# Performance work log

Measured on AMD Instinct MI355X. Metric: run time of the kernel, lower is better.

The kernel has to match this reference:

```python
import jax, jax.numpy as jnp
import numpy as np

IH, IW = 32, 32
HEADS = 8
DIM_HEAD = 64
SCALE = DIM_HEAD ** -0.5


def _make_relative_index():
    # Matches torch buffer: ceil Euclidean distance between all pairs of 2D coords.
    ii, jj = np.meshgrid(np.arange(IH), np.arange(IW), indexing='ij')
    coords = np.stack([ii.ravel(), jj.ravel()])  # [2, n]
    rel = coords[:, :, None] - coords[:, None, :]  # [2, n, n]
    dist = np.ceil(np.sqrt(rel[0] ** 2 + rel[1] ** 2))
    return jnp.asarray(dist.astype(np.int32).ravel())  # [n*n]


def setup_inputs() -> dict:
    key = jax.random.key(0)
    k1, k2, k3, k4 = jax.random.split(key, 4)
    b, n, inp = 32, IH * IW, 512
    inner = HEADS * DIM_HEAD
    diag = int(np.ceil(np.sqrt((IH - 1) ** 2 + (IW - 1) ** 2)))
    return {
        'x': jax.random.normal(k1, (b, n, inp), jnp.float32),
        'w_qkv': jax.random.normal(k2, (inp, inner * 3), jnp.float32) * (inp ** -0.5),
        'bias_table': jax.random.normal(k3, (diag + 1, HEADS), jnp.float32) * 0.02,
        'w_out': jax.random.normal(k4, (inner, 512), jnp.float32) * (inner ** -0.5),
        'b_out': jnp.zeros((512,), jnp.float32),
        'relative_index': _make_relative_index(),
    }


def reference(x, w_qkv, bias_table, w_out, b_out, relative_index):
    b, n, _ = x.shape
    qkv = x @ w_qkv  # [b, n, 3*inner]
    q, k, v = jnp.split(qkv, 3, axis=-1)
    def to_heads(t):
        return t.reshape(b, n, HEADS, DIM_HEAD).transpose(0, 2, 1, 3)  # b h n d
    q, k, v = to_heads(q), to_heads(k), to_heads(v)
    dots = jnp.einsum('bhid,bhjd->bhij', q, k) * SCALE  # [b, h, n, n]
    # gather relative bias: [n*n, h] -> [1, h, n, n]
    rel_bias = bias_table[relative_index].reshape(n, n, HEADS).transpose(2, 0, 1)
    attn = jax.nn.softmax(dots + rel_bias[None], axis=-1)
    out = jnp.einsum('bhij,bhjd->bhid', attn, v)  # b h n d
    out = out.transpose(0, 2, 1, 3).reshape(b, n, HEADS * DIM_HEAD)
    return out @ w_out + b_out
```

## Files before the change

### kernel.cpp

```cpp
#include <hip/hip_runtime.h>
#include <hip/hip_bf16.h>
#include <cstdint>

typedef __bf16 bf16_t;
typedef bf16_t bf16x8 __attribute__((ext_vector_type(8)));
typedef float f32x4 __attribute__((ext_vector_type(4)));
typedef float f32x16 __attribute__((ext_vector_type(16)));
typedef unsigned u32x4 __attribute__((ext_vector_type(4)));

#define MFMA16(a, b, c) __builtin_amdgcn_mfma_f32_16x16x32_bf16(a, b, c, 0, 0, 0)
#define MFMA32(a, b, c) __builtin_amdgcn_mfma_f32_32x32x16_bf16(a, b, c, 0, 0, 0)

#define GLOAD_LDS16(g, l)                                                  \
    __builtin_amdgcn_global_load_lds(                                      \
        (const __attribute__((address_space(1))) unsigned*)(g),            \
        (__attribute__((address_space(3))) unsigned*)(l), 16, 0, 0)

constexpr int LDK = 72;

#define QSCALE 0.1803368801f
#define LOG2E 1.44269504f

__global__ void zero_out(unsigned short* __restrict__ out, long n) {
    long i = (long)blockIdx.x * 256 + threadIdx.x;
    if (i < n) out[i] = 0;
}

__global__ void detect_dtype(const unsigned* __restrict__ x,
                             int* __restrict__ flag) {
    if (threadIdx.x == 0 && blockIdx.x == 0) {
        int cnt = 0;
        for (int i = 0; i < 1024; ++i) {
            unsigned e = (x[i] >> 7) & 0xFF;
            cnt += (e > 100 && e < 150) ? 1 : 0;
        }
        *flag = (cnt > 512) ? 1 : 0;
    }
}

__global__ __launch_bounds__(256) void convert_x(const void* __restrict__ in,
                                                 bf16_t* __restrict__ out,
                                                 const int* __restrict__ flagp) {
    const int fl = *flagp;
    long i = ((long)blockIdx.x * 256 + threadIdx.x) * 8;
    if (fl) {
        *(bf16x8*)&out[i] = *(const bf16x8*)&((const bf16_t*)in)[i];
    } else {
        f32x4 lo = *(const f32x4*)&((const float*)in)[i];
        f32x4 hi = *(const f32x4*)&((const float*)in)[i + 4];
        bf16x8 v;
#pragma unroll
        for (int e = 0; e < 4; ++e) {
            v[e] = (bf16_t)lo[e];
            v[e + 4] = (bf16_t)hi[e];
        }
        *(bf16x8*)&out[i] = v;
    }
}

__global__ void transpose_flex(const void* __restrict__ in,
                               bf16_t* __restrict__ out, int R, int C,
                               const int* __restrict__ flagp, int scale_rows) {
    const int fl = *flagp;
    __shared__ bf16_t tile[32][33];
    int c0 = blockIdx.x * 32, r0 = blockIdx.y * 32;
    int x = threadIdx.x, y = threadIdx.y;
#pragma unroll
    for (int i = 0; i < 4; ++i) {
        long idx = (long)(r0 + y + 8 * i) * C + c0 + x;
        float fv = fl ? (float)((const bf16_t*)in)[idx]
                      : ((const float*)in)[idx];
        if (c0 + x < scale_rows) fv *= QSCALE;
        tile[y + 8 * i][x] = (bf16_t)fv;
    }
    __syncthreads();
#pragma unroll
    for (int i = 0; i < 4; ++i)
        out[(long)(c0 + y + 8 * i) * R + r0 + x] = tile[x][y + 8 * i];
}

__global__ __launch_bounds__(256) void build_bias_perm(
    const int* __restrict__ rel_index, const void* __restrict__ bias_table,
    float* __restrict__ perm, const int* __restrict__ flagp) {
    const int fl = *flagp;
    const int jt = blockIdx.x;
    const int qb = blockIdx.y;
    const int t = threadIdx.x;
    const int lane = t & 63;
    const int h = (t >> 6) + 4 * blockIdx.z;
    const int i = qb * 32 + (lane & 31);
    const int hi = lane >> 5;
    float out[16];
#pragma unroll
    for (int r = 0; r < 16; ++r) {
        int j = jt * 32 + (r & 3) + 8 * (r >> 2) + 4 * hi;
        int ridx = rel_index[i * 1024 + j];
        ridx = ridx < 0 ? 0 : (ridx > 44 ? 44 : ridx);
        float bv = fl ? (float)((const bf16_t*)bias_table)[ridx * 8 + h]
                      : ((const float*)bias_table)[ridx * 8 + h];
        out[r] = bv * LOG2E;
    }
    long off = (((long)(h * 32 + qb) * 32 + jt) << 10) + lane * 16;
#pragma unroll
    for (int g = 0; g < 4; ++g)
        *(f32x4*)&perm[off + 4 * g] = *(f32x4*)&out[4 * g];
}

__global__ __launch_bounds__(256) void transpose_v(
    const bf16_t* __restrict__ qkv, bf16_t* __restrict__ vt) {
    __shared__ bf16_t tile[64 * 64];
    const int jt = blockIdx.x;
    const int bh = blockIdx.y;
    const int b = bh >> 3, h = bh & 7;
    const bf16_t* src = qkv + (long)b * 1024 * 1536 + 1024 + h * 64;
    const int t = threadIdx.x;
    const int r = t >> 3, c8 = t & 7;
    const int j0 = jt * 64;
#pragma unroll
    for (int rep = 0; rep < 2; ++rep) {
        int jj = r + 32 * rep;
        *(bf16x8*)&tile[jj * 64 + ((c8 ^ (jj >> 3)) << 3)] =
            *(const bf16x8*)&src[(long)(j0 + jj) * 1536 + c8 * 8];
    }
    __syncthreads();
#pragma unroll
    for (int rep = 0; rep < 2; ++rep) {
        int dd = r + 32 * rep;
        int jc = c8 * 8;
        bf16_t o[8];
#pragma unroll
        for (int e = 0; e < 8; ++e) {
            int row = jc + e;
            o[e] = tile[row * 64 + (((dd >> 3) ^ (row >> 3)) << 3) + (dd & 7)];
        }
        *(bf16x8*)&vt[((long)bh << 16) + (long)dd * 1024 + j0 + jc] =
            *(bf16x8*)&o[0];
    }
}

template <bool BIAS, bool OUTFLEX>
__global__ __launch_bounds__(256) void gemm_lds(
    const bf16_t* __restrict__ A, const bf16_t* __restrict__ Bt, int K,
    int lda, long a_row0, void* __restrict__ C, int ldc, long c_row0,
    const void* __restrict__ bias, const int* __restrict__ flagp) {
    const int fl = *flagp;
    __shared__ bf16_t a_lds[128 * 64];
    __shared__ bf16_t b_lds[128 * 64];
    int t = threadIdx.x;
    int wave = t >> 6, lane = t & 63;
    int m16 = lane & 15, quad = lane >> 4;
    int wr = wave >> 1, wc = wave & 1;
    long m0 = (long)blockIdx.y * 128;
    int n0 = blockIdx.x * 128;

    f32x4 acc[4][4] = {};

    for (int ks = 0; ks < K; ks += 64) {
#pragma unroll
        for (int i = 0; i < 4; ++i) {
            int c = wave * 256 + i * 64 + lane;
            int row = c >> 3, kc = (c & 7) << 3;
            GLOAD_LDS16(&A[(a_row0 + m0 + row) * (long)lda + ks + kc],
                        &a_lds[row * 64 + kc]);
            GLOAD_LDS16(&Bt[(long)(n0 + row) * K + ks + kc],
                        &b_lds[row * 64 + kc]);
        }
        __syncthreads();
#pragma unroll
        for (int kf = 0; kf < 2; ++kf) {
            bf16x8 af[4], bfr[4];
#pragma unroll
            for (int mb = 0; mb < 4; ++mb)
                af[mb] = *(const bf16x8*)&a_lds[(wr * 64 + mb * 16 + m16) * 64 +
                                                kf * 32 + quad * 8];
#pragma unroll
            for (int nb = 0; nb < 4; ++nb)
                bfr[nb] = *(const bf16x8*)&b_lds[(wc * 64 + nb * 16 + m16) * 64 +
                                                 kf * 32 + quad * 8];
#pragma unroll
            for (int mb = 0; mb < 4; ++mb)
#pragma unroll
                for (int nb = 0; nb < 4; ++nb)
                    acc[mb][nb] = MFMA16(af[mb], bfr[nb], acc[mb][nb]);
        }
        __syncthreads();
    }

#pragma unroll
    for (int mb = 0; mb < 4; ++mb) {
#pragma unroll
        for (int nb = 0; nb < 4; ++nb) {
            int col = n0 + wc * 64 + nb * 16 + m16;
#pragma unroll
            for (int r = 0; r < 4; ++r) {
                long row = m0 + wr * 64 + mb * 16 + quad * 4 + r;
                float v = acc[mb][nb][r];
                if (BIAS) {
                    float bb = fl ? (float)((const bf16_t*)bias)[col]
                                  : ((const float*)bias)[col];
                    v += bb;
                }
                long off = (c_row0 + row) * (long)ldc + col;
                if (OUTFLEX && !fl)
                    ((float*)C)[off] = v;
                else
                    ((bf16_t*)C)[off] = (bf16_t)v;
            }
        }
    }
}

template <bool AFLEX, bool BIAS, bool OUTFLEX>
__global__ __launch_bounds__(256) void gemm128(
    const void* __restrict__ A, const bf16_t* __restrict__ Bt, int K, int lda,
    long a_row0, void* __restrict__ C, int ldc, long c_row0,
    const void* __restrict__ bias, const int* __restrict__ flagp) {
    const int fl = *flagp;
    __shared__ bf16_t a_lds[128 * LDK];
    __shared__ bf16_t b_lds[128 * LDK];
    int t = threadIdx.x;
    int wave = t >> 6, lane = t & 63;
    int m16 = lane & 15, quad = lane >> 4;
    int wr = wave >> 1, wc = wave & 1;
    long m0 = (long)blockIdx.y * 128;
    int n0 = blockIdx.x * 128;

    f32x4 acc[4][4] = {};

    for (int ks = 0; ks < K; ks += 64) {
#pragma unroll
        for (int i = 0; i < 4; ++i) {
            int c = t + 256 * i;
            int row = c >> 3;
            int kc = (c & 7) << 3;
            bf16x8 av;
            if (AFLEX && !fl) {
                const float* Af = (const float*)A;
                long base = (a_row0 + m0 + row) * (long)lda + ks + kc;
                f32x4 lo = *(const f32x4*)&Af[base];
                f32x4 hi = *(const f32x4*)&Af[base + 4];
#pragma unroll
                for (int e = 0; e < 4; ++e) {
                    av[e] = (bf16_t)lo[e];
                    av[e + 4] = (bf16_t)hi[e];
                }
            } else {
                av = *(const bf16x8*)&(
                    (const bf16_t*)A)[(a_row0 + m0 + row) * (long)lda + ks + kc];
            }
            *(bf16x8*)&a_lds[row * LDK + kc] = av;
            *(bf16x8*)&b_lds[row * LDK + kc] =
                *(const bf16x8*)&Bt[(long)(n0 + row) * K + ks + kc];
        }
        __syncthreads();
#pragma unroll
        for (int kf = 0; kf < 2; ++kf) {
            bf16x8 af[4], bfr[4];
#pragma unroll
            for (int mb = 0; mb < 4; ++mb)
                af[mb] = *(const bf16x8*)&a_lds[(wr * 64 + mb * 16 + m16) * LDK +
                                                kf * 32 + quad * 8];
#pragma unroll
            for (int nb = 0; nb < 4; ++nb)
                bfr[nb] = *(const bf16x8*)&b_lds[(wc * 64 + nb * 16 + m16) * LDK +
                                                 kf * 32 + quad * 8];
#pragma unroll
            for (int mb = 0; mb < 4; ++mb)
#pragma unroll
                for (int nb = 0; nb < 4; ++nb)
                    acc[mb][nb] = MFMA16(af[mb], bfr[nb], acc[mb][nb]);
        }
        __syncthreads();
    }

#pragma unroll
    for (int mb = 0; mb < 4; ++mb) {
#pragma unroll
        for (int nb = 0; nb < 4; ++nb) {
            int col = n0 + wc * 64 + nb * 16 + m16;
#pragma unroll
            for (int r = 0; r < 4; ++r) {
                long row = m0 + wr * 64 + mb * 16 + quad * 4 + r;
                float v = acc[mb][nb][r];
                if (BIAS) {
                    float bb = fl ? (float)((const bf16_t*)bias)[col]
                                  : ((const float*)bias)[col];
                    v += bb;
                }
                long off = (c_row0 + row) * (long)ldc + col;
                if (OUTFLEX && !fl)
                    ((float*)C)[off] = v;
                else
                    ((bf16_t*)C)[off] = (bf16_t)v;
            }
        }
    }
}

__global__ __launch_bounds__(256, 2) void flash_attn3(
    bf16_t* __restrict__ qkv, const bf16_t* __restrict__ vt,
    const float* __restrict__ bias_perm) {
    __shared__ bf16_t k_lds[2][64 * 64];
    __shared__ bf16_t v_lds[2][64 * 64];

    const int t = threadIdx.x;
    const int lane = t & 63, wave = t >> 6;
    const int l31 = lane & 31, hi = lane >> 5;
    const int h = blockIdx.x;
    const int b = blockIdx.z;
    bf16_t* base = qkv + (long)b * 1024 * 1536;
    bf16_t* qb = base + h * 64;
    const bf16_t* kb = base + 512 + h * 64;
    const bf16_t* vtb = vt + ((long)(b * 8 + h) << 16);
    const int qblkA = blockIdx.y * 4 + wave;
    const int qblkB = qblkA + 16;
    const int q0A = qblkA * 32, q0B = qblkB * 32;
    const float* bpA = bias_perm + (((long)(h * 32 + qblkA)) << 15) + lane * 16;
    const float* bpB = bias_perm + (((long)(h * 32 + qblkB)) << 15) + lane * 16;

    bf16x8 qfA[4], qfB[4];
#pragma unroll
    for (int s = 0; s < 4; ++s) {
        qfA[s] = *(const bf16x8*)&qb[(long)(q0A + l31) * 1536 + s * 16 + hi * 8];
        qfB[s] = *(const bf16x8*)&qb[(long)(q0B + l31) * 1536 + s * 16 + hi * 8];
    }

    f32x16 oacc0A = {}, oacc1A = {}, laccA = {};
    f32x16 oacc0B = {}, oacc1B = {}, laccB = {};
    bf16x8 ones;
#pragma unroll
    for (int e = 0; e < 8; ++e) ones[e] = (bf16_t)1.0f;

    const int srow = t >> 3, pc = t & 7;
    const int kc0 = (pc ^ (srow & 7)) << 3;

    {
        GLOAD_LDS16(&kb[(long)srow * 1536 + kc0],
                    &k_lds[0][srow * 64 + pc * 8]);
        GLOAD_LDS16(&kb[(long)(srow + 32) * 1536 + kc0],
                    &k_lds[0][(srow + 32) * 64 + pc * 8]);
        GLOAD_LDS16(&vtb[(long)srow * 1024 + kc0],
                    &v_lds[0][srow * 64 + pc * 8]);
        GLOAD_LDS16(&vtb[(long)(srow + 32) * 1024 + kc0],
                    &v_lds[0][(srow + 32) * 64 + pc * 8]);
    }
    __syncthreads();

#define SOFTMAX_REPACK(S, DW)                                              \
    {                                                                      \
        float sv_[16];                                                     \
        _Pragma("unroll") for (int r = 0; r < 16; ++r)                     \
            sv_[r] = __builtin_amdgcn_exp2f((S)[r]);                       \
        _Pragma("unroll") for (int g = 0; g < 4; ++g) {                    \
            unsigned da_, db_;                                             \
            asm("v_cvt_pk_bf16_f32 %0, %1, %2"                             \
                : "=v"(da_) : "v"(sv_[4 * g]), "v"(sv_[4 * g + 1]));       \
            asm("v_cvt_pk_bf16_f32 %0, %1, %2"                             \
                : "=v"(db_) : "v"(sv_[4 * g + 2]), "v"(sv_[4 * g + 3]));   \
            (DW)[2 * g] = da_;                                             \
            (DW)[2 * g + 1] = db_;                                         \
        }                                                                  \
        _Pragma("unroll") for (int kk = 0; kk < 2; ++kk) {                 \
            asm("v_permlane32_swap_b32 %0, %1"                             \
                : "+v"((DW)[4 * kk + 0]), "+v"((DW)[4 * kk + 2]));         \
            asm("v_permlane32_swap_b32 %0, %1"                             \
                : "+v"((DW)[4 * kk + 1]), "+v"((DW)[4 * kk + 3]));         \
        }                                                                  \
    }

#define PACK_PA(DW, KK)                                                    \
    __builtin_bit_cast(bf16x8, (u32x4){(DW)[4 * (KK) + 0],                 \
                                       (DW)[4 * (KK) + 1],                 \
                                       (DW)[4 * (KK) + 2],                 \
                                       (DW)[4 * (KK) + 3]})

    for (int tt = 0; tt < 16; ++tt) {
        const int cur = tt & 1;
        const float* btA = bpA + ((long)tt << 11);
        const float* btB = bpB + ((long)tt << 11);
        f32x4 bA0[4], bB0[4];
#pragma unroll
        for (int g = 0; g < 4; ++g) {
            bA0[g] = *(const f32x4*)(btA + 4 * g);
            bB0[g] = *(const f32x4*)(btB + 4 * g);
        }
        if (tt < 15) {
            const int nb = cur ^ 1;
            long j0n = (long)(tt + 1) * 64;
            GLOAD_LDS16(&kb[(j0n + srow) * 1536 + kc0],
                        &k_lds[nb][srow * 64 + pc * 8]);
            GLOAD_LDS16(&kb[(j0n + srow + 32) * 1536 + kc0],
                        &k_lds[nb][(srow + 32) * 64 + pc * 8]);
            GLOAD_LDS16(&vtb[(long)srow * 1024 + j0n + kc0],
                        &v_lds[nb][srow * 64 + pc * 8]);
            GLOAD_LDS16(&vtb[(long)(srow + 32) * 1024 + j0n + kc0],
                        &v_lds[nb][(srow + 32) * 64 + pc * 8]);
        }

        f32x4 bA1[4], bB1[4];
#pragma unroll
        for (int js = 0; js < 2; ++js) {
            const int krow = js * 32 + l31;
            bf16x8 kf[4];
#pragma unroll
            for (int st = 0; st < 4; ++st)
                kf[st] = *(const bf16x8*)&k_lds[cur][krow * 64 +
                          (((st * 2 + hi) ^ (krow & 7)) << 3)];
            f32x16 sA, sB;
#pragma unroll
            for (int g = 0; g < 4; ++g) {
                const f32x4 ba = js ? bA1[g] : bA0[g];
                const f32x4 bb = js ? bB1[g] : bB0[g];
#pragma unroll
                for (int e = 0; e < 4; ++e) {
                    sA[4 * g + e] = ba[e];
                    sB[4 * g + e] = bb[e];
                }
            }
            __builtin_amdgcn_s_setprio(1);
#pragma unroll
            for (int st = 0; st < 4; ++st) sA = MFMA32(kf[st], qfA[st], sA);
#pragma unroll
            for (int st = 0; st < 4; ++st) sB = MFMA32(kf[st], qfB[st], sB);
            __builtin_amdgcn_s_setprio(0);
            if (js == 0) {
#pragma unroll
                for (int g = 0; g < 4; ++g) {
                    bA1[g] = *(const f32x4*)(btA + 1024 + 4 * g);
                    bB1[g] = *(const f32x4*)(btB + 1024 + 4 * g);
                }
            }
            unsigned dwA[8], dwB[8];
            SOFTMAX_REPACK(sA, dwA);
            SOFTMAX_REPACK(sB, dwB);
            __builtin_amdgcn_s_setprio(1);
#pragma unroll
            for (int kk = 0; kk < 2; ++kk) {
                bf16x8 paA = PACK_PA(dwA, kk);
                bf16x8 paB = PACK_PA(dwB, kk);
                const int vr0 = l31, vr1 = 32 + l31;
                bf16x8 vf0 = *(const bf16x8*)&v_lds[cur][vr0 * 64 +
                              (((js * 4 + kk * 2 + hi) ^ (vr0 & 7)) << 3)];
                bf16x8 vf1 = *(const bf16x8*)&v_lds[cur][vr1 * 64 +
                              (((js * 4 + kk * 2 + hi) ^ (vr1 & 7)) << 3)];
                laccA = MFMA32(paA, ones, laccA);
                oacc0A = MFMA32(paA, vf0, oacc0A);
                oacc1A = MFMA32(paA, vf1, oacc1A);
                laccB = MFMA32(paB, ones, laccB);
                oacc0B = MFMA32(paB, vf0, oacc0B);
                oacc1B = MFMA32(paB, vf1, oacc1B);
            }
            __builtin_amdgcn_s_setprio(0);
        }
        __syncthreads();
    }

#pragma unroll
    for (int r = 0; r < 16; ++r) {
        int row = (r & 3) + 8 * (r >> 2) + 4 * hi;
        float invA = 1.0f / laccA[r];
        float invB = 1.0f / laccB[r];
        qb[(long)(q0A + row) * 1536 + l31] = (bf16_t)(oacc0A[r] * invA);
        qb[(long)(q0A + row) * 1536 + 32 + l31] = (bf16_t)(oacc1A[r] * invA);
        qb[(long)(q0B + row) * 1536 + l31] = (bf16_t)(oacc0B[r] * invB);
        qb[(long)(q0B + row) * 1536 + 32 + l31] = (bf16_t)(oacc1B[r] * invB);
    }
}

__global__ __launch_bounds__(256) void flash_attn2(
    bf16_t* __restrict__ qkv, const float* __restrict__ bias_perm) {
    __shared__ bf16_t k_lds[2][64 * 64];
    __shared__ bf16_t v_lds[2][64 * 64];

    const int t = threadIdx.x;
    const int lane = t & 63, wave = t >> 6;
    const int l31 = lane & 31, hi = lane >> 5;
    const int h = blockIdx.x;
    const int b = blockIdx.z;
    bf16_t* base = qkv + (long)b * 1024 * 1536;
    bf16_t* qb = base + h * 64;
    const bf16_t* kb = base + 512 + h * 64;
    const bf16_t* vb = base + 1024 + h * 64;
    const int qblk = blockIdx.y * 4 + wave;
    const int q0w = qblk * 32;
    const float* bp = bias_perm + (((long)(h * 32 + qblk)) << 15) + lane * 16;

    bf16x8 qf[4];
#pragma unroll
    for (int s = 0; s < 4; ++s)
        qf[s] = *(const bf16x8*)&qb[(long)(q0w + l31) * 1536 + s * 16 + hi * 8];

    f32x16 oacc0 = {}, oacc1 = {}, lacc = {};
    bf16x8 ones;
#pragma unroll
    for (int e = 0; e < 8; ++e) ones[e] = (bf16_t)1.0f;

    const int sr0 = t >> 3, sg0 = t & 7;
    const int sr1 = sr0 + 32;

    {
        bf16x8 k0 = *(const bf16x8*)&kb[(long)sr0 * 1536 + sg0 * 8];
        bf16x8 k1 = *(const bf16x8*)&kb[(long)sr1 * 1536 + sg0 * 8];
        bf16x8 v0 = *(const bf16x8*)&vb[(long)sr0 * 1536 + sg0 * 8];
        bf16x8 v1 = *(const bf16x8*)&vb[(long)sr1 * 1536 + sg0 * 8];
        *(bf16x8*)&k_lds[0][sr0 * 64 + ((sg0 ^ (sr0 & 7)) << 3)] = k0;
        *(bf16x8*)&k_lds[0][sr1 * 64 + ((sg0 ^ (sr1 & 7)) << 3)] = k1;
#pragma unroll
        for (int e = 0; e < 8; ++e) {
            int d0 = sg0 * 8 + e;
            v_lds[0][d0 * 64 + (((sr0 >> 3) ^ (d0 & 7)) << 3) + (sr0 & 7)] = v0[e];
            v_lds[0][d0 * 64 + (((sr1 >> 3) ^ (d0 & 7)) << 3) + (sr1 & 7)] = v1[e];
        }
    }
    __syncthreads();

    for (int tt = 0; tt < 16; ++tt) {
        const int cur = tt & 1;
        bf16x8 kn0 = {}, kn1 = {}, vn0 = {}, vn1 = {};
        if (tt < 15) {
            long j0n = (long)(tt + 1) * 64;
            kn0 = *(const bf16x8*)&kb[(j0n + sr0) * 1536 + sg0 * 8];
            kn1 = *(const bf16x8*)&kb[(j0n + sr1) * 1536 + sg0 * 8];
            vn0 = *(const bf16x8*)&vb[(j0n + sr0) * 1536 + sg0 * 8];
            vn1 = *(const bf16x8*)&vb[(j0n + sr1) * 1536 + sg0 * 8];
        }
        const float* bt = bp + ((long)tt << 11);
        f32x4 bv[8];
        bv[0] = *(const f32x4*)(bt);
        bv[1] = *(const f32x4*)(bt + 4);
        bv[2] = *(const f32x4*)(bt + 8);
        bv[3] = *(const f32x4*)(bt + 12);
        bv[4] = *(const f32x4*)(bt + 1024);
        bv[5] = *(const f32x4*)(bt + 1028);
        bv[6] = *(const f32x4*)(bt + 1032);
        bv[7] = *(const f32x4*)(bt + 1036);

#pragma unroll
        for (int js = 0; js < 2; ++js) {
            f32x16 s;
#pragma unroll
            for (int g = 0; g < 4; ++g) {
#pragma unroll
                for (int e = 0; e < 4; ++e) s[4 * g + e] = bv[4 * js + g][e];
            }
            const int krow = js * 32 + l31;
#pragma unroll
            for (int st = 0; st < 4; ++st) {
                bf16x8 kf = *(const bf16x8*)&k_lds[cur][krow * 64 +
                             (((st * 2 + hi) ^ (krow & 7)) << 3)];
                s = MFMA32(kf, qf[st], s);
            }
            float sv[16];
#pragma unroll
            for (int r = 0; r < 16; ++r)
                sv[r] = __builtin_amdgcn_exp2f(s[r]);
            unsigned dw[8];
#pragma unroll
            for (int g = 0; g < 4; ++g) {
                unsigned da, db;
                asm("v_cvt_pk_bf16_f32 %0, %1, %2"
                    : "=v"(da) : "v"(sv[4 * g]), "v"(sv[4 * g + 1]));
                asm("v_cvt_pk_bf16_f32 %0, %1, %2"
                    : "=v"(db) : "v"(sv[4 * g + 2]), "v"(sv[4 * g + 3]));
                dw[2 * g] = da;
                dw[2 * g + 1] = db;
            }
#pragma unroll
            for (int kk = 0; kk < 2; ++kk) {
                asm("v_permlane32_swap_b32 %0, %1"
                    : "+v"(dw[4 * kk + 0]), "+v"(dw[4 * kk + 2]));
                asm("v_permlane32_swap_b32 %0, %1"
                    : "+v"(dw[4 * kk + 1]), "+v"(dw[4 * kk + 3]));
            }
#pragma unroll
            for (int kk = 0; kk < 2; ++kk) {
                u32x4 uv;
                uv[0] = dw[4 * kk + 0];
                uv[1] = dw[4 * kk + 1];
                uv[2] = dw[4 * kk + 2];
                uv[3] = dw[4 * kk + 3];
                bf16x8 pa = __builtin_bit_cast(bf16x8, uv);
                lacc = MFMA32(pa, ones, lacc);
#pragma unroll
                for (int db2 = 0; db2 < 2; ++db2) {
                    const int vrow = db2 * 32 + l31;
                    bf16x8 vf = *(const bf16x8*)&v_lds[cur][vrow * 64 +
                                 (((js * 4 + kk * 2 + hi) ^ (vrow & 7)) << 3)];
                    if (db2 == 0)
                        oacc0 = MFMA32(pa, vf, oacc0);
                    else
                        oacc1 = MFMA32(pa, vf, oacc1);
                }
            }
        }
        if (tt < 15) {
            const int nb = cur ^ 1;
            *(bf16x8*)&k_lds[nb][sr0 * 64 + ((sg0 ^ (sr0 & 7)) << 3)] = kn0;
            *(bf16x8*)&k_lds[nb][sr1 * 64 + ((sg0 ^ (sr1 & 7)) << 3)] = kn1;
#pragma unroll
            for (int e = 0; e < 8; ++e) {
                int d0 = sg0 * 8 + e;
                v_lds[nb][d0 * 64 + (((sr0 >> 3) ^ (d0 & 7)) << 3) + (sr0 & 7)] =
                    vn0[e];
                v_lds[nb][d0 * 64 + (((sr1 >> 3) ^ (d0 & 7)) << 3) + (sr1 & 7)] =
                    vn1[e];
            }
        }
        __syncthreads();
    }

#pragma unroll
    for (int r = 0; r < 16; ++r) {
        float inv = 1.0f / lacc[r];
        int row = (r & 3) + 8 * (r >> 2) + 4 * hi;
        qb[(long)(q0w + row) * 1536 + l31] = (bf16_t)(oacc0[r] * inv);
        qb[(long)(q0w + row) * 1536 + 32 + l31] = (bf16_t)(oacc1[r] * inv);
    }
}

extern "C" void kernel_launch(void* const* d_in, const int* in_sizes, int n_in,
                              void* d_out, int out_size, void* d_ws,
                              size_t ws_size, hipStream_t stream) {
    const void* x = nullptr;
    const void* w_qkv = nullptr;
    const void* bias_table = nullptr;
    const void* w_out = nullptr;
    const void* b_out = nullptr;
    const void* rel_raw = nullptr;
    for (int i = 0; i < n_in; ++i) {
        switch (in_sizes[i]) {
            case 16777216: x = d_in[i]; break;
            case 786432:  w_qkv = d_in[i]; break;
            case 360:     bias_table = d_in[i]; break;
            case 262144:  w_out = d_in[i]; break;
            case 512:     b_out = d_in[i]; break;
            case 1048576: rel_raw = d_in[i]; break;
            default: break;
        }
    }
    if (!x || !w_qkv || !bias_table || !w_out || !b_out || !rel_raw) {
        x = d_in[0]; w_qkv = d_in[1]; bias_table = d_in[2];
        w_out = d_in[3]; b_out = d_in[4]; rel_raw = d_in[5];
    }
    const int* rel_index = (const int*)rel_raw;

    char* ws = (char*)d_ws;
    bf16_t* wqkvT = (bf16_t*)ws;
    bf16_t* woutT = (bf16_t*)(ws + 1572864);
    int* flag = (int*)(ws + 1572864 + 524288);
    float* rel_bias = (float*)(ws + 1572864 + 524288 + 256);
    const size_t fixed = 1572864 + 524288 + 256 + 33554432;
    const size_t xbf_bytes = (size_t)32 * 1024 * 512 * sizeof(bf16_t);
    const size_t qkv_pb = (size_t)1024 * 1536 * sizeof(bf16_t);
    const size_t vt_pb = (size_t)8 * 64 * 1024 * sizeof(bf16_t);

    if (ws_size < fixed + qkv_pb) {
        long n = (long)out_size;
        long nblk = (n + 255) / 256;
        if (nblk > 0)
            zero_out<<<(unsigned)nblk, 256, 0, stream>>>(
                (unsigned short*)d_out, n);
        return;
    }

    bool have_xbf = ws_size >= fixed + xbf_bytes + qkv_pb;
    bool have_vt = ws_size >= fixed + xbf_bytes + qkv_pb + vt_pb;
    bf16_t* x_bf = (bf16_t*)(ws + fixed);
    bf16_t* qkv = have_xbf ? (bf16_t*)(ws + fixed + xbf_bytes)
                           : (bf16_t*)(ws + fixed);

    size_t avail = ws_size - fixed - (have_xbf ? xbf_bytes : 0);
    size_t pb = have_vt ? (qkv_pb + vt_pb) : qkv_pb;
    int chunk = (int)(avail / pb);
    if (chunk > 32) chunk = 32;
    if (chunk < 1) chunk = 1;
    while (32 % chunk) --chunk;
    bf16_t* vt = (bf16_t*)((char*)qkv + (size_t)chunk * qkv_pb);

    detect_dtype<<<1, 64, 0, stream>>>((const unsigned*)x, flag);
    transpose_flex<<<dim3(1536 / 32, 512 / 32), dim3(32, 8), 0, stream>>>(
        w_qkv, wqkvT, 512, 1536, flag, 512);
    transpose_flex<<<dim3(512 / 32, 512 / 32), dim3(32, 8), 0, stream>>>(
        w_out, woutT, 512, 512, flag, 0);
    build_bias_perm<<<dim3(32, 32, 2), 256, 0, stream>>>(
        rel_index, bias_table, rel_bias, flag);
    if (have_xbf)
        convert_x<<<8192, 256, 0, stream>>>(x, x_bf, flag);

    for (int b0 = 0; b0 < 32; b0 += chunk) {
        long row0 = (long)b0 * 1024;
        int mrows = chunk * 1024;
        if (have_xbf) {
            gemm_lds<false, false>
                <<<dim3(1536 / 128, mrows / 128), 256, 0, stream>>>(
                    x_bf, wqkvT, 512, 512, row0, qkv, 1536, 0, nullptr, flag);
        } else {
            gemm128<true, false, false>
                <<<dim3(1536 / 128, mrows / 128), 256, 0, stream>>>(
                    x, wqkvT, 512, 512, row0, qkv, 1536, 0, nullptr, flag);
        }
        if (have_vt) {
            transpose_v<<<dim3(16, chunk * 8), 256, 0, stream>>>(qkv, vt);
            flash_attn3<<<dim3(8, 4, chunk), 256, 0, stream>>>(qkv, vt,
                                                               rel_bias);
        } else {
            flash_attn2<<<dim3(8, 8, chunk), 256, 0, stream>>>(qkv, rel_bias);
        }
        gemm_lds<true, true>
            <<<dim3(512 / 128, mrows / 128), 256, 0, stream>>>(
                qkv, woutT, 512, 1536, 0, d_out, 512, row0, b_out, flag);
    }
}
```

Baseline: 461.9 us.

## Fuse V transpose into QKV GEMM epilogue and triple-buffer attention K/V loads

The QKV projection GEMM now writes the V columns directly in transposed layout into the vt buffer, which removes the separate transpose_v kernel and its extra read/write pass over V. The flash attention kernel moves from a double-buffered to a triple-buffered K/V LDS pipeline: it prefetches two tiles ahead, uses raw s_waitcnt/s_barrier instead of __syncthreads, and hoists the second-half bias loads. It also drops the occupancy hint of 2 blocks per CU. The larger LDS footprint and the missing occupancy hint may cut blocks per CU, and the uint2 transposed stores from the GEMM epilogue are narrow and strided.

```diff
diff --git a/kernel.cpp b/kernel.cpp
--- a/kernel.cpp
+++ b/kernel.cpp
@@ -106,43 +106,12 @@
         *(f32x4*)&perm[off + 4 * g] = *(f32x4*)&out[4 * g];
 }
 
-__global__ __launch_bounds__(256) void transpose_v(
-    const bf16_t* __restrict__ qkv, bf16_t* __restrict__ vt) {
-    __shared__ bf16_t tile[64 * 64];
-    const int jt = blockIdx.x;
-    const int bh = blockIdx.y;
-    const int b = bh >> 3, h = bh & 7;
-    const bf16_t* src = qkv + (long)b * 1024 * 1536 + 1024 + h * 64;
-    const int t = threadIdx.x;
-    const int r = t >> 3, c8 = t & 7;
-    const int j0 = jt * 64;
-#pragma unroll
-    for (int rep = 0; rep < 2; ++rep) {
-        int jj = r + 32 * rep;
-        *(bf16x8*)&tile[jj * 64 + ((c8 ^ (jj >> 3)) << 3)] =
-            *(const bf16x8*)&src[(long)(j0 + jj) * 1536 + c8 * 8];
-    }
-    __syncthreads();
-#pragma unroll
-    for (int rep = 0; rep < 2; ++rep) {
-        int dd = r + 32 * rep;
-        int jc = c8 * 8;
-        bf16_t o[8];
-#pragma unroll
-        for (int e = 0; e < 8; ++e) {
-            int row = jc + e;
-            o[e] = tile[row * 64 + (((dd >> 3) ^ (row >> 3)) << 3) + (dd & 7)];
-        }
-        *(bf16x8*)&vt[((long)bh << 16) + (long)dd * 1024 + j0 + jc] =
-            *(bf16x8*)&o[0];
-    }
-}
-
-template <bool BIAS, bool OUTFLEX>
+template <bool BIAS, bool OUTFLEX, bool VSPLIT>
 __global__ __launch_bounds__(256) void gemm_lds(
     const bf16_t* __restrict__ A, const bf16_t* __restrict__ Bt, int K,
     int lda, long a_row0, void* __restrict__ C, int ldc, long c_row0,
-    const void* __restrict__ bias, const int* __restrict__ flagp) {
+    const void* __restrict__ bias, bf16_t* __restrict__ vtout,
+    const int* __restrict__ flagp) {
     const int fl = *flagp;
     __shared__ bf16_t a_lds[128 * 64];
     __shared__ bf16_t b_lds[128 * 64];
@@ -191,20 +160,33 @@
 #pragma unroll
         for (int nb = 0; nb < 4; ++nb) {
             int col = n0 + wc * 64 + nb * 16 + m16;
-#pragma unroll
-            for (int r = 0; r < 4; ++r) {
-                long row = m0 + wr * 64 + mb * 16 + quad * 4 + r;
-                float v = acc[mb][nb][r];
-                if (BIAS) {
-                    float bb = fl ? (float)((const bf16_t*)bias)[col]
-                                  : ((const float*)bias)[col];
-                    v += bb;
+            long rowb = m0 + wr * 64 + mb * 16 + quad * 4;
+            if (VSPLIT && col >= 1024) {
+                int dd = col - 1024;
+                bf16_t ov[4];
+#pragma unroll
+                for (int r = 0; r < 4; ++r) ov[r] = (bf16_t)acc[mb][nb][r];
+                long bb_ = rowb >> 10;
+                long jj = rowb & 1023;
+                *(uint2*)&vtout[((bb_ * 8 + (dd >> 6)) << 16) +
+                                (long)(dd & 63) * 1024 + jj] =
+                    *(const uint2*)&ov[0];
+            } else {
+#pragma unroll
+                for (int r = 0; r < 4; ++r) {
+                    long row = rowb + r;
+                    float v = acc[mb][nb][r];
+                    if (BIAS) {
+                        float bb = fl ? (float)((const bf16_t*)bias)[col]
+                                      : ((const float*)bias)[col];
+                        v += bb;
+                    }
+                    long off = (c_row0 + row) * (long)ldc + col;
+                    if (OUTFLEX && !fl)
+                        ((float*)C)[off] = v;
+                    else
+                        ((bf16_t*)C)[off] = (bf16_t)v;
                 }
-                long off = (c_row0 + row) * (long)ldc + col;
-                if (OUTFLEX && !fl)
-                    ((float*)C)[off] = v;
-                else
-                    ((bf16_t*)C)[off] = (bf16_t)v;
             }
         }
     }
@@ -297,11 +279,11 @@
     }
 }
 
-__global__ __launch_bounds__(256, 2) void flash_attn3(
+__global__ __launch_bounds__(256) void flash_attn3(
     bf16_t* __restrict__ qkv, const bf16_t* __restrict__ vt,
     const float* __restrict__ bias_perm) {
-    __shared__ bf16_t k_lds[2][64 * 64];
-    __shared__ bf16_t v_lds[2][64 * 64];
+    __shared__ bf16_t k_lds[3][64 * 64];
+    __shared__ bf16_t v_lds[3][64 * 64];
 
     const int t = threadIdx.x;
     const int lane = t & 63, wave = t >> 6;
@@ -334,17 +316,21 @@
     const int srow = t >> 3, pc = t & 7;
     const int kc0 = (pc ^ (srow & 7)) << 3;
 
-    {
-        GLOAD_LDS16(&kb[(long)srow * 1536 + kc0],
-                    &k_lds[0][srow * 64 + pc * 8]);
-        GLOAD_LDS16(&kb[(long)(srow + 32) * 1536 + kc0],
-                    &k_lds[0][(srow + 32) * 64 + pc * 8]);
-        GLOAD_LDS16(&vtb[(long)srow * 1024 + kc0],
-                    &v_lds[0][srow * 64 + pc * 8]);
-        GLOAD_LDS16(&vtb[(long)(srow + 32) * 1024 + kc0],
-                    &v_lds[0][(srow + 32) * 64 + pc * 8]);
-    }
-    __syncthreads();
+#define STAGE_TILE(BUF, J0)                                                \
+    {                                                                      \
+        GLOAD_LDS16(&kb[((J0) + srow) * 1536 + kc0],                       \
+                    &k_lds[BUF][srow * 64 + pc * 8]);                      \
+        GLOAD_LDS16(&kb[((J0) + srow + 32) * 1536 + kc0],                  \
+                    &k_lds[BUF][(srow + 32) * 64 + pc * 8]);               \
+        GLOAD_LDS16(&vtb[(long)srow * 1024 + (J0) + kc0],                  \
+                    &v_lds[BUF][srow * 64 + pc * 8]);                      \
+        GLOAD_LDS16(&vtb[(long)(srow + 32) * 1024 + (J0) + kc0],           \
+                    &v_lds[BUF][(srow + 32) * 64 + pc * 8]);               \
+    }
+
+    STAGE_TILE(0, (long)0);
+    STAGE_TILE(1, (long)64);
+    asm volatile("s_waitcnt vmcnt(4)\n\ts_barrier" ::: "memory");
 
 #define SOFTMAX_REPACK(S, DW)                                              \
     {                                                                      \
@@ -375,29 +361,28 @@
                                        (DW)[4 * (KK) + 3]})
 
     for (int tt = 0; tt < 16; ++tt) {
-        const int cur = tt & 1;
+        const int cur = tt % 3;
         const float* btA = bpA + ((long)tt << 11);
         const float* btB = bpB + ((long)tt << 11);
-        f32x4 bA0[4], bB0[4];
+        f32x4 bA0[4], bB0[4], bA1[4], bB1[4];
 #pragma unroll
         for (int g = 0; g < 4; ++g) {
             bA0[g] = *(const f32x4*)(btA + 4 * g);
             bB0[g] = *(const f32x4*)(btB + 4 * g);
         }
-        if (tt < 15) {
-            const int nb = cur ^ 1;
-            long j0n = (long)(tt + 1) * 64;
-            GLOAD_LDS16(&kb[(j0n + srow) * 1536 + kc0],
-                        &k_lds[nb][srow * 64 + pc * 8]);
-            GLOAD_LDS16(&kb[(j0n + srow + 32) * 1536 + kc0],
-                        &k_lds[nb][(srow + 32) * 64 + pc * 8]);
-            GLOAD_LDS16(&vtb[(long)srow * 1024 + j0n + kc0],
-                        &v_lds[nb][srow * 64 + pc * 8]);
-            GLOAD_LDS16(&vtb[(long)(srow + 32) * 1024 + j0n + kc0],
-                        &v_lds[nb][(srow + 32) * 64 + pc * 8]);
-        }
-
-        f32x4 bA1[4], bB1[4];
+#pragma unroll
+        for (int g = 0; g < 4; ++g) {
+            bA1[g] = *(const f32x4*)(btA + 1024 + 4 * g);
+            bB1[g] = *(const f32x4*)(btB + 1024 + 4 * g);
+        }
+        __builtin_amdgcn_sched_barrier(0);
+        {
+            const long td = (tt + 2 < 16) ? (long)(tt + 2) * 64 : (long)15 * 64;
+            const int nb = (tt + 2) % 3;
+            STAGE_TILE(nb, td);
+        }
+        __builtin_amdgcn_sched_barrier(0);
+
 #pragma unroll
         for (int js = 0; js < 2; ++js) {
             const int krow = js * 32 + l31;
@@ -423,13 +408,6 @@
 #pragma unroll
             for (int st = 0; st < 4; ++st) sB = MFMA32(kf[st], qfB[st], sB);
             __builtin_amdgcn_s_setprio(0);
-            if (js == 0) {
-#pragma unroll
-                for (int g = 0; g < 4; ++g) {
-                    bA1[g] = *(const f32x4*)(btA + 1024 + 4 * g);
-                    bB1[g] = *(const f32x4*)(btB + 1024 + 4 * g);
-                }
-            }
             unsigned dwA[8], dwB[8];
             SOFTMAX_REPACK(sA, dwA);
             SOFTMAX_REPACK(sB, dwB);
@@ -452,8 +430,10 @@
             }
             __builtin_amdgcn_s_setprio(0);
         }
-        __syncthreads();
-    }
+
+        asm volatile("s_barrier" ::: "memory");
+    }
+    asm volatile("s_waitcnt vmcnt(0)" ::: "memory");
 
 #pragma unroll
     for (int r = 0; r < 16; ++r) {
@@ -664,7 +644,7 @@
     }
 
     bool have_xbf = ws_size >= fixed + xbf_bytes + qkv_pb;
-    bool have_vt = ws_size >= fixed + xbf_bytes + qkv_pb + vt_pb;
+    bool have_vt = have_xbf && (ws_size >= fixed + xbf_bytes + qkv_pb + vt_pb);
     bf16_t* x_bf = (bf16_t*)(ws + fixed);
     bf16_t* qkv = have_xbf ? (bf16_t*)(ws + fixed + xbf_bytes)
                            : (bf16_t*)(ws + fixed);
@@ -691,23 +671,31 @@
         long row0 = (long)b0 * 1024;
         int mrows = chunk * 1024;
         if (have_xbf) {
-            gemm_lds<false, false>
-                <<<dim3(1536 / 128, mrows / 128), 256, 0, stream>>>(
-                    x_bf, wqkvT, 512, 512, row0, qkv, 1536, 0, nullptr, flag);
+            if (have_vt) {
+                gemm_lds<false, false, true>
+                    <<<dim3(1536 / 128, mrows / 128), 256, 0, stream>>>(
+                        x_bf, wqkvT, 512, 512, row0, qkv, 1536, 0, nullptr,
+                        vt, flag);
+            } else {
+                gemm_lds<false, false, false>
+                    <<<dim3(1536 / 128, mrows / 128), 256, 0, stream>>>(
+                        x_bf, wqkvT, 512, 512, row0, qkv, 1536, 0, nullptr,
+                        nullptr, flag);
+            }
         } else {
             gemm128<true, false, false>
                 <<<dim3(1536 / 128, mrows / 128), 256, 0, stream>>>(
                     x, wqkvT, 512, 512, row0, qkv, 1536, 0, nullptr, flag);
         }
         if (have_vt) {
-            transpose_v<<<dim3(16, chunk * 8), 256, 0, stream>>>(qkv, vt);
             flash_attn3<<<dim3(8, 4, chunk), 256, 0, stream>>>(qkv, vt,
                                                                rel_bias);
         } else {
             flash_attn2<<<dim3(8, 8, chunk), 256, 0, stream>>>(qkv, rel_bias);
         }
-        gemm_lds<true, true>
+        gemm_lds<true, true, false>
             <<<dim3(512 / 128, mrows / 128), 256, 0, stream>>>(
-                qkv, woutT, 512, 1536, 0, d_out, 512, row0, b_out, flag);
-    }
-}
+                qkv, woutT, 512, 1536, 0, d_out, 512, row0, b_out,
+                nullptr, flag);
+    }
+}
```

Measured after the change: 531.2 us. +15.0%, slower.
